# Optimization experiments

Measured on AMD Instinct MI355X. Metric: run time of the kernel, lower is better.

Reference implementation:

```python
import jax, jax.numpy as jnp
import numpy as np
from jax.scipy.special import logsumexp


def setup_inputs() -> dict:
    key = jax.random.key(0)
    B, C, H, W = 2, 32, 128, 128
    sizes = [(H, W)] + [(H // 2, W // 2)] * 4
    ks = iter(jax.random.split(key, 32))
    inp = {}
    for t, (hh, ww) in enumerate(sizes):
        inp[f"unary_h{t}"] = jax.random.normal(next(ks), (B, C, hh, ww), jnp.float32)
        inp[f"unary_v{t}"] = jax.random.normal(next(ks), (B, C, hh, ww), jnp.float32)
        inp[f"pairwise_h{t}"] = 0.1 * jax.random.normal(next(ks), (B, C, C, hh, ww - 1), jnp.float32)
        inp[f"pairwise_v{t}"] = 0.1 * jax.random.normal(next(ks), (B, C, C, hh - 1, ww), jnp.float32)
    inp["gamma"] = jnp.ones((1,), jnp.float32)
    return inp


def _chain_marginals(unary, pairwise, gamma):
    """Entropy-smoothed max-product marginals along the LAST axis.
    unary: [B,C,L,T], pairwise: [B,C,C,L,T-1] (pairwise[b,i,j,l,t] couples state i at t with j at t+1).
    Returns soft marginals [B,C,L,T] (softmax over C per position)."""
    u = jnp.transpose(unary, (3, 0, 2, 1))        # [T,B,L,C]
    pw = jnp.transpose(pairwise, (4, 0, 3, 1, 2))  # [T-1,B,L,C,C]
    inv_g = 1.0 / gamma

    def fwd_step(f, xs):
        u_t, pw_t = xs
        f_new = u_t + gamma * logsumexp(f[..., :, None] * inv_g + pw_t * inv_g, axis=-2)
        return f_new, f_new

    _, f_rest = jax.lax.scan(fwd_step, u[0], (u[1:], pw))
    f = jnp.concatenate([u[:1], f_rest], axis=0)

    def bwd_step(bb, xs):
        u_t, pw_t = xs
        b_new = u_t + gamma * logsumexp(bb[..., None, :] * inv_g + pw_t * inv_g, axis=-1)
        return b_new, b_new

    _, b_rest = jax.lax.scan(bwd_step, u[-1], (u[:-1][::-1], pw[::-1]))
    b = jnp.concatenate([u[-1:], b_rest], axis=0)[::-1]

    marg = jax.nn.softmax((f + b - u) * inv_g, axis=-1)  # [T,B,L,C]
    return jnp.transpose(marg, (1, 3, 2, 0))             # [B,C,L,T]


def _dp_pair(uh, uv, ph, pv, g):
    # horizontal chains (along W) with unary_h, vertical chains (along H) with unary_v
    mh = _chain_marginals(uh, ph, g)
    mv = _chain_marginals(uv.swapaxes(2, 3), pv.swapaxes(3, 4), g).swapaxes(2, 3)
    return mh, mv


def _scatter_up(m, stride, i, j, H, W):
    # max_unpool2d with the structured indices: m[y,x] -> (i + y*stride, j + x*stride), then crop/pad to (H,W)
    b, c, h_, w_ = m.shape
    up = jnp.zeros((b, c, h_ * stride, w_ * stride), m.dtype).at[:, :, i::stride, j::stride].set(m)
    up = up[:, :, :H, :W]
    ph, pw = H - up.shape[2], W - up.shape[3]
    if ph > 0 or pw > 0:
        up = jnp.pad(up, ((0, 0), (0, 0), (0, max(ph, 0)), (0, max(pw, 0))))
    return up


def reference(unary_h0, unary_h1, unary_h2, unary_h3, unary_h4,
              unary_v0, unary_v1, unary_v2, unary_v3, unary_v4,
              pairwise_h0, pairwise_h1, pairwise_h2, pairwise_h3, pairwise_h4,
              pairwise_v0, pairwise_v1, pairwise_v2, pairwise_v3, pairwise_v4,
              gamma):
    uh = [unary_h0, unary_h1, unary_h2, unary_h3, unary_h4]
    uv = [unary_v0, unary_v1, unary_v2, unary_v3, unary_v4]
    ph = [pairwise_h0, pairwise_h1, pairwise_h2, pairwise_h3, pairwise_h4]
    pv = [pairwise_v0, pairwise_v1, pairwise_v2, pairwise_v3, pairwise_v4]
    g = jnp.clip(gamma.reshape(()), 0.01)  # learned gamma, clamped min 0.01

    H, W = uh[0].shape[2], uh[0].shape[3]
    alpha = 1.0 / W if W > H else 1.0 / H

    mh0, mv0 = _dp_pair(uh[0], uv[0], ph[0], pv[0], g)
    marg_hs, marg_vs = [mh0], [mv0]
    mh_acc, mv_acc = mh0, mv0

    stride, cnt = 2, 1  # step_size = 1 default -> one extra scale with a 2x2 shifted grid
    for i in range(stride):
        for j in range(stride):
            m_h, m_v = _dp_pair(uh[cnt], uv[cnt], ph[cnt], pv[cnt], g)
            marg_hs.append(m_h)
            marg_vs.append(m_v)
            mh_acc = mh_acc + _scatter_up(m_h, stride, i, j, H, W)
            mv_acc = mv_acc + _scatter_up(m_v, stride, i, j, H, W)
            cnt += 1

    num_pairwise_terms = 2
    avg = (mh_acc + mv_acc) / (num_pairwise_terms * 2)

    new_uh0 = uh[0] - alpha * (marg_hs[0] - avg)
    new_uv0 = uv[0] - alpha * (marg_vs[0] - avg)
    # fine-scale unary updates (computed for faithfulness; gradients flow through avg)
    cnt = 1
    new_uh_fine, new_uv_fine = [], []
    for i in range(stride):
        for j in range(stride):
            new_uh_fine.append(uh[cnt] - alpha * (marg_hs[cnt] - avg[:, :, i::stride, j::stride]))
            new_uv_fine.append(uv[cnt] - alpha * (marg_vs[cnt] - avg[:, :, i::stride, j::stride]))
            cnt += 1

    main = jnp.stack([new_uh0, new_uv0, mh_acc, mv_acc], axis=0)  # [4,B,C,H,W]
    return main
```

## Files before the change

### kernel.cpp

```cpp
#include <hip/hip_runtime.h>
#include <stdint.h>

#define TC 2
#define CHUNK_BYTES 4096
#define CHUNK_F4 256

static __device__ __forceinline__ float lse16x2(const float* v, float igl2, float gln2, float uval)
{
  float a0=fmaxf(v[0],v[8]), a1=fmaxf(v[1],v[9]), a2=fmaxf(v[2],v[10]), a3=fmaxf(v[3],v[11]);
  float a4=fmaxf(v[4],v[12]),a5=fmaxf(v[5],v[13]),a6=fmaxf(v[6],v[14]),a7=fmaxf(v[7],v[15]);
  float b0=fmaxf(a0,a4), b1=fmaxf(a1,a5), b2=fmaxf(a2,a6), b3=fmaxf(a3,a7);
  float m = fmaxf(fmaxf(b0,b1), fmaxf(b2,b3));
  float e0 = exp2f((v[0]-m)*igl2) + exp2f((v[1]-m)*igl2);
  float e1 = exp2f((v[2]-m)*igl2) + exp2f((v[3]-m)*igl2);
  float e2 = exp2f((v[4]-m)*igl2) + exp2f((v[5]-m)*igl2);
  float e3 = exp2f((v[6]-m)*igl2) + exp2f((v[7]-m)*igl2);
  float e4 = exp2f((v[8]-m)*igl2) + exp2f((v[9]-m)*igl2);
  float e5 = exp2f((v[10]-m)*igl2) + exp2f((v[11]-m)*igl2);
  float e6 = exp2f((v[12]-m)*igl2) + exp2f((v[13]-m)*igl2);
  float e7 = exp2f((v[14]-m)*igl2) + exp2f((v[15]-m)*igl2);
  float s = ((e0+e1)+(e2+e3)) + ((e4+e5)+(e6+e7));
  float mo = __shfl_xor(m, 32);
  float m2 = fmaxf(m, mo);
  float sadj = s * exp2f((m - m2) * igl2);
  float stot = sadj + __shfl_xor(sadj, 32);
  return uval + m2 + gln2 * __log2f(stot);
}

static __device__ __forceinline__ float softmax32(float z)
{
  float zm = z;
  zm = fmaxf(zm, __shfl_xor(zm, 16));
  zm = fmaxf(zm, __shfl_xor(zm, 8));
  zm = fmaxf(zm, __shfl_xor(zm, 4));
  zm = fmaxf(zm, __shfl_xor(zm, 2));
  zm = fmaxf(zm, __shfl_xor(zm, 1));
  float p = exp2f((z - zm) * 1.4426950408889634f);
  float ps = p;
  ps += __shfl_xor(ps, 16);
  ps += __shfl_xor(ps, 8);
  ps += __shfl_xor(ps, 4);
  ps += __shfl_xor(ps, 2);
  ps += __shfl_xor(ps, 1);
  return p / ps;
}

static __device__ __forceinline__ uint32_t pkbf(float a, float b)
{
  uint32_t ua = __float_as_uint(a), ub = __float_as_uint(b);
  ua = (ua + 0x7FFFu + ((ua >> 16) & 1u)) >> 16;
  ub = (ub + 0x7FFFu + ((ub >> 16) & 1u)) & 0xFFFF0000u;
  return ua | ub;
}

struct TSeg { const float* pw; uint16_t* PT; int L, Tt, Tpad, fStride, Xtot, dirV, blockBase, nx, ny; };
struct TTable { TSeg s[10]; int nseg; };
struct USeg { const float* U; float* Ut; int fs, nx, ny, L, T, dirV, blockBase; };
struct UTable { USeg s[10]; int nseg; };
struct DSeg { const uint16_t* PT; const float* Ut; float* F; float* B; int chainBase, T, Tt, Tpad; };
struct DTable { DSeg s[10]; int nseg; };
struct MSeg { const float* F; const float* B; const float* Ut; float* out; int L, T, dirV, blockBase, nrx, nfx; };
struct MTable { MSeg s[10]; int nseg; };

__global__ __launch_bounds__(256) void k_transpose_all(TTable tbl)
{
  __shared__ uint16_t tile[128][128];
  int bid = blockIdx.x;
  int k = 0;
  for (int q = 1; q < tbl.nseg; q++) if (bid >= tbl.s[q].blockBase) k = q;
  TSeg sg = tbl.s[k];
  int r = bid - sg.blockBase;
  int jg = r & 7; r >>= 3;
  int w = r % sg.nx; int tmp = r / sg.nx;
  int fixed = tmp % sg.ny;
  int b = tmp / sg.ny;
  int j0 = jg * 4;
  int g = fixed * sg.fStride;
  int a = g & 31;
  int xbase = w * 128 - a;
  if (xbase >= sg.Xtot) return;
  int tid = threadIdx.x;
  int kx = tid & 31, psub = tid >> 5;
  int pstride = sg.L * sg.Tt;
  int clampMax = 2048 * pstride - 4;
  int jthr = j0 + (psub & 3);
  int swj = (jthr >> 1) & 3;
  int gp0 = ((psub >> 2) << 5) + jthr;
  int idx0 = ((b << 10) + gp0) * pstride + (g - a) + (w << 7) + (kx << 2);
  const float* pw = sg.pw;
  #pragma unroll
  for (int hp = 0; hp < 2; hp++) {
    float4 st[8];
    #pragma unroll
    for (int q = 0; q < 8; q++) {
      int batch = hp * 8 + q;
      int idx = idx0 + batch * (pstride << 6);
      idx = idx > clampMax ? clampMax : idx;
      st[q] = *(const float4*)(pw + idx);
    }
    #pragma unroll
    for (int q = 0; q < 8; q++) {
      int batch = hp * 8 + q;
      int i = 2 * batch + (psub >> 2);
      int sw = swj ^ (((i >> 3) & 3) << 2);
      int pl = batch * 8 + psub;
      uint32_t pk0 = pkbf(st[q].x, st[q].y);
      uint32_t pk1 = pkbf(st[q].z, st[q].w);
      if (sw & 1) { uint32_t tswp = pk0; pk0 = pk1; pk1 = tswp; }
      *(uint2*)((unsigned char*)tile + pl * 256 + 8 * (kx ^ (sw >> 1))) = make_uint2(pk0, pk1);
    }
  }
  __syncthreads();
  uint32_t* PTd = (uint32_t*)sg.PT;
  #pragma unroll
  for (int w8 = 0; w8 < 8; w8++) {
    int gidx = w8 * 256 + tid;
    int xs = gidx >> 4;
    int q = gidx & 15;
    int xv = xbase + xs;
    if (xv < 0 || xv >= sg.Xtot) continue;
    int jl = q >> 2, j = j0 + jl;
    int perm3 = (j >> 1) & 7;
    int swjW = (j >> 1) & 3;
    uint32_t pk[4];
    #pragma unroll
    for (int e = 0; e < 4; e++) {
      int wd = ((q & 3) << 2) + e;
      int pos = wd >> 1, pr = wd & 1;
      int i0 = ((pos ^ perm3) << 2) + pr * 2;
      int sw = swjW ^ (((i0 >> 3) & 3) << 2);
      int c = (xs >> 1) ^ sw;
      int u16c = (c << 1) | (xs & 1);
      int r0 = (i0 << 2) + jl;
      uint32_t v0 = tile[r0][u16c];
      uint32_t v1 = tile[r0 + 4][u16c];
      pk[e] = v0 | (v1 << 16);
    }
    int chain, tsl;
    if (sg.dirV) { chain = b * sg.Xtot + xv; tsl = fixed; }
    else         { chain = b * sg.ny + fixed; tsl = xv; }
    *(uint4*)&PTd[((size_t)chain * sg.Tpad + tsl) * 512 + j * 16 + (q & 3) * 4] =
        make_uint4(pk[0], pk[1], pk[2], pk[3]);
  }
}

__global__ __launch_bounds__(256) void k_ut_all(UTable tbl)
{
  __shared__ float tile[32][33];
  int bid = blockIdx.x;
  int k = 0;
  for (int q = 1; q < tbl.nseg; q++) if (bid >= tbl.s[q].blockBase) k = q;
  USeg sg = tbl.s[k];
  int r = bid - sg.blockBase;
  int bx = r % sg.nx; int tmp = r / sg.nx;
  int fixed = tmp % sg.ny;
  int b = tmp / sg.ny;
  int tid = threadIdx.x;
  size_t LT = (size_t)sg.L * sg.T;
  int x0 = bx * 32;
  int xx = tid & 31;
  #pragma unroll
  for (int it = 0; it < 4; it++) {
    int c = (tid >> 5) + it * 8;
    tile[xx][c] = sg.U[(size_t)b * 32 * LT + (size_t)c * LT + (size_t)fixed * sg.fs + x0 + xx];
  }
  __syncthreads();
  int xw = tid >> 3;
  int ci = (tid & 7) * 4;
  int chain = sg.dirV ? b * sg.L + x0 + xw : b * sg.L + fixed;
  int tIdx  = sg.dirV ? fixed : x0 + xw;
  float4 vv = make_float4(tile[xw][ci], tile[xw][ci + 1], tile[xw][ci + 2], tile[xw][ci + 3]);
  *(float4*)&sg.Ut[((size_t)chain * sg.T + tIdx) * 32 + ci] = vv;
}

__global__ __launch_bounds__(64) void k_dp_all(DTable tbl, const float* __restrict__ gamma, int nDP)
{
  __shared__ __align__(16) unsigned char lds[2 * CHUNK_BYTES + 1024];
  float* f_out = (float*)(lds + 2 * CHUNK_BYTES);
  int bid = blockIdx.x;
  int isB = (bid >= nDP) ? 1 : 0;
  bid -= isB * nDP;
  int k = 0;
  for (int q = 1; q < tbl.nseg; q++) if (bid >= tbl.s[q].chainBase) k = q;
  DSeg sg = tbl.s[k];
  int chain = bid - sg.chainBase;
  int T = sg.T, Tt = sg.Tt;
  int tid = threadIdx.x, j = tid & 31, h = tid >> 5;
  float g = fmaxf(gamma[0], 0.01f);
  float igl2 = (1.0f / g) * 1.4426950408889634f;
  float gln2 = g * 0.6931471805599453f;
  const float* Utc = sg.Ut + (size_t)chain * T * 32;
  float* Oc = (isB ? sg.B : sg.F) + (size_t)chain * T * 32;
  const float4* src = (const float4*)(sg.PT + (size_t)chain * sg.Tpad * 1024);
  int nch = sg.Tpad / TC;
  int perm3 = (j >> 1) & 7;
  int gbase = h * 48;
  float4 stg[4];
  if (!isB) {
    float cur = Utc[j];
    if (h == 0) f_out[j] = cur;
    #pragma unroll
    for (int q = 0; q < 4; q++) stg[q] = src[q * 64 + tid];
    int buf = 0;
    for (int ch = 0; ch < nch; ch++) {
      float4* dst = (float4*)(lds + buf * CHUNK_BYTES);
      #pragma unroll
      for (int q = 0; q < 4; q++) dst[q * 64 + tid] = stg[q];
      if (ch + 1 < nch) {
        const float4* s2 = src + (size_t)(ch + 1) * CHUNK_F4;
        #pragma unroll
        for (int q = 0; q < 4; q++) stg[q] = s2[q * 64 + tid];
      }
      #pragma unroll
      for (int ss = 0; ss < TC; ss++) {
        int s = ch * TC + ss;
        if (s >= Tt) break;
        const uint32_t* sl = (const uint32_t*)(lds + buf * CHUNK_BYTES + ss * 2048);
        float v[16];
        #pragma unroll
        for (int rr = 0; rr < 4; rr++) {
          int pos = (4 * h + rr) ^ perm3;
          uint2 dv = *(const uint2*)&sl[j * 16 + pos * 2];
          v[rr * 4 + 0] = __uint_as_float(dv.x << 16);
          v[rr * 4 + 1] = __uint_as_float(dv.x & 0xFFFF0000u);
          v[rr * 4 + 2] = __uint_as_float(dv.y << 16);
          v[rr * 4 + 3] = __uint_as_float(dv.y & 0xFFFF0000u);
        }
        #pragma unroll
        for (int q = 0; q < 16; q++) v[q] += __shfl(cur, gbase + q);
        int t = s + 1;
        float uval = Utc[(size_t)t * 32 + j];
        cur = lse16x2(v, igl2, gln2, uval);
        if (h == 0) f_out[(t & 7) * 32 + j] = cur;
        if ((t & 7) == 7) {
          float4 vv = *(float4*)&f_out[tid * 4];
          *(float4*)&Oc[(size_t)(t - 7) * 32 + tid * 4] = vv;
        }
      }
      buf ^= 1;
    }
  } else {
    int p2i = j >> 2, pri = (j >> 1) & 1, loi = j & 1;
    float cur = Utc[(size_t)(T - 1) * 32 + j];
    if (h == 0) f_out[7 * 32 + j] = cur;
    {
      const float4* s2 = src + (size_t)(nch - 1) * CHUNK_F4;
      #pragma unroll
      for (int q = 0; q < 4; q++) stg[q] = s2[q * 64 + tid];
    }
    int buf = 0;
    for (int ch = nch - 1; ch >= 0; ch--) {
      float4* dst = (float4*)(lds + buf * CHUNK_BYTES);
      #pragma unroll
      for (int q = 0; q < 4; q++) dst[q * 64 + tid] = stg[q];
      if (ch > 0) {
        const float4* s2 = src + (size_t)(ch - 1) * CHUNK_F4;
        #pragma unroll
        for (int q = 0; q < 4; q++) stg[q] = s2[q * 64 + tid];
      }
      #pragma unroll
      for (int ss = TC - 1; ss >= 0; ss--) {
        int s = ch * TC + ss;
        if (s >= Tt) continue;
        const uint16_t* row16 = (const uint16_t*)(lds + buf * CHUNK_BYTES + ss * 2048);
        float v[16];
        #pragma unroll
        for (int jj = 0; jj < 16; jj++) {
          int u16idx = (16 * h + jj) * 32 + ((p2i ^ (jj >> 1)) * 2 + pri) * 2 + loi;
          v[jj] = __uint_as_float((uint32_t)row16[u16idx] << 16);
        }
        #pragma unroll
        for (int q = 0; q < 16; q++) v[q] += __shfl(cur, gbase + q);
        float uval = Utc[(size_t)s * 32 + j];
        cur = lse16x2(v, igl2, gln2, uval);
        if (h == 0) f_out[(s & 7) * 32 + j] = cur;
        if ((s & 7) == 0) {
          float4 vv = *(float4*)&f_out[tid * 4];
          *(float4*)&Oc[(size_t)s * 32 + tid * 4] = vv;
        }
      }
      buf ^= 1;
    }
  }
}

__global__ __launch_bounds__(256) void k_marg_all(MTable tbl, const float* __restrict__ gamma)
{
  __shared__ float sm[32][33];
  int bid = blockIdx.x;
  int k = 0;
  for (int q = 1; q < tbl.nseg; q++) if (bid >= tbl.s[q].blockBase) k = q;
  MSeg sg = tbl.s[k];
  int r = bid - sg.blockBase;
  int rx = r % sg.nrx; int tmp = r / sg.nrx;
  int fx = tmp % sg.nfx; int b = tmp / sg.nfx;
  int tid = threadIdx.x;
  float g = fmaxf(gamma[0], 0.01f);
  float ig = 1.0f / g;
  int c = tid & 31;
  int L = sg.L, T = sg.T;
  size_t LT = (size_t)L * T;
  int RA = sg.dirV ? L : T;
  int r0 = rx * 32;
  #pragma unroll
  for (int pass = 0; pass < 4; pass++) {
    int rr = (tid >> 5) + pass * 8;
    int rowAxis = r0 + rr;
    int chain = sg.dirV ? b * L + rowAxis : b * L + fx;
    int t = sg.dirV ? fx : rowAxis;
    size_t idx = ((size_t)chain * T + t) * 32 + c;
    float z = (sg.F[idx] + sg.B[idx] - sg.Ut[idx]) * ig;
    sm[rr][c] = softmax32(z);
  }
  __syncthreads();
  int cc = tid >> 3;
  int xl = (tid & 7) * 4;
  size_t obase = (size_t)b * 32 * LT + (size_t)fx * RA + r0;
  float4 vv = make_float4(sm[xl][cc], sm[xl + 1][cc], sm[xl + 2][cc], sm[xl + 3][cc]);
  *(float4*)&sg.out[obase + (size_t)cc * LT + xl] = vv;
}

__global__ __launch_bounds__(256) void k_combine(
    const float* __restrict__ uh0, const float* __restrict__ uv0,
    const float* __restrict__ MB, float* __restrict__ out)
{
  int t4 = blockIdx.x * 256 + threadIdx.x;
  int base = t4 * 4;
  int x = base & 127, y = (base >> 7) & 127;
  int bc = base >> 14;
  float4 mh0 = *(const float4*)&MB[base];
  float4 mv0 = *(const float4*)&MB[1048576 + base];
  int ce = 1 + ((y & 1) << 1);
  int coff = bc * 4096 + ((y >> 1) << 6) + (x >> 1);
  const float* cbE = MB + 2097152 + (size_t)(ce - 1) * 524288;
  const float* cbO = cbE + 524288;
  float2 mhcE = *(const float2*)&cbE[coff];
  float2 mhcO = *(const float2*)&cbO[coff];
  float2 mvcE = *(const float2*)&cbE[262144 + coff];
  float2 mvcO = *(const float2*)&cbO[262144 + coff];
  float4 u_h = *(const float4*)&uh0[base];
  float4 u_v = *(const float4*)&uv0[base];
  float mh[4] = {mh0.x, mh0.y, mh0.z, mh0.w};
  float mv[4] = {mv0.x, mv0.y, mv0.z, mv0.w};
  float uh[4] = {u_h.x, u_h.y, u_h.z, u_h.w};
  float uv[4] = {u_v.x, u_v.y, u_v.z, u_v.w};
  float mhc[4] = {mhcE.x, mhcO.x, mhcE.y, mhcO.y};
  float mvc[4] = {mvcE.x, mvcO.x, mvcE.y, mvcO.y};
  float o0[4], o1[4], o2[4], o3[4];
  const float A = 0.0078125f;
  #pragma unroll
  for (int e = 0; e < 4; e++) {
    float mha = mh[e] + mhc[e], mva = mv[e] + mvc[e];
    float avg = (mha + mva) * 0.25f;
    o0[e] = uh[e] - A * (mh[e] - avg);
    o1[e] = uv[e] - A * (mv[e] - avg);
    o2[e] = mha; o3[e] = mva;
  }
  *(float4*)&out[base]           = make_float4(o0[0], o0[1], o0[2], o0[3]);
  *(float4*)&out[1048576 + base] = make_float4(o1[0], o1[1], o1[2], o1[3]);
  *(float4*)&out[2097152 + base] = make_float4(o2[0], o2[1], o2[2], o2[3]);
  *(float4*)&out[3145728 + base] = make_float4(o3[0], o3[1], o3[2], o3[3]);
}

static void fill_tseg(TSeg& t, const float* pw, uint16_t* PT, int L, int T, int dirV, int blockBase)
{
  int Tt = T - 1;
  t.pw = pw; t.PT = PT;
  t.L = L; t.Tt = Tt; t.Tpad = T;
  t.fStride = dirV ? L : Tt;
  t.Xtot = dirV ? L : Tt;
  t.dirV = dirV;
  int pad = (t.fStride & 31) ? 31 : 0;
  t.nx = (t.Xtot + pad + 127) / 128;
  t.ny = dirV ? Tt : L;
  t.blockBase = blockBase;
}

extern "C" void kernel_launch(void* const* d_in, const int* in_sizes, int n_in,
                              void* d_out, int out_size, void* d_ws, size_t ws_size,
                              hipStream_t stream)
{
  (void)in_sizes; (void)n_in; (void)out_size;
  const float* gamma = (const float*)d_in[20];
  unsigned char* ws = (unsigned char*)d_ws;

  int segL[10], segT[10];
  const float* segPW[10]; const float* segUU[10];
  size_t segMG[10];
  for (int lvl = 0; lvl < 5; lvl++) {
    int H = lvl ? 64 : 128, W = H;
    int si = lvl * 2;
    segL[si] = H; segT[si] = W;
    segPW[si] = (const float*)d_in[lvl * 4 + 2];
    segUU[si] = (const float*)d_in[lvl * 4 + 0];
    segL[si + 1] = W; segT[si + 1] = H;
    segPW[si + 1] = (const float*)d_in[lvl * 4 + 3];
    segUU[si + 1] = (const float*)d_in[lvl * 4 + 1];
    if (lvl == 0) { segMG[0] = 0; segMG[1] = 1048576; }
    else { segMG[si] = 2097152 + (size_t)(lvl - 1) * 524288; segMG[si + 1] = segMG[si] + 262144; }
  }

  const size_t NEED = 318767104ull;
  if (ws_size >= NEED) {
    uint16_t* PT0 = (uint16_t*)ws;
    float* MARG = (float*)ws;
    float* F0  = (float*)(ws + 268435456ull);
    float* B0  = (float*)(ws + 285212672ull);
    float* Ut0 = (float*)(ws + 301989888ull);

    TTable tt; UTable ut; DTable dt; MTable mt;
    tt.nseg = 10; ut.nseg = 10; dt.nseg = 10; mt.nseg = 10;
    size_t ptOff = 0, fuOff = 0;
    int tB = 0, uB = 0, cB = 0, mB = 0;
    for (int s = 0; s < 10; s++) {
      int dirV = s & 1;
      int L = segL[s], T = segT[s];
      int chains = 2 * L;
      fill_tseg(tt.s[s], segPW[s], PT0 + ptOff, L, T, dirV, tB);
      tB += 2 * tt.s[s].ny * tt.s[s].nx * 8;
      USeg& u = ut.s[s];
      u.U = segUU[s]; u.Ut = Ut0 + fuOff;
      u.fs = dirV ? L : T;
      u.nx = (dirV ? L : T) / 32;
      u.ny = dirV ? T : L;
      u.L = L; u.T = T; u.dirV = dirV;
      u.blockBase = uB;
      uB += u.nx * u.ny * 2;
      DSeg& d = dt.s[s];
      d.PT = PT0 + ptOff; d.Ut = Ut0 + fuOff;
      d.F = F0 + fuOff; d.B = B0 + fuOff;
      d.chainBase = cB; d.T = T; d.Tt = T - 1; d.Tpad = T;
      cB += chains;
      MSeg& m = mt.s[s];
      m.F = F0 + fuOff; m.B = B0 + fuOff; m.Ut = Ut0 + fuOff;
      m.out = MARG + segMG[s];
      m.L = L; m.T = T; m.dirV = dirV;
      m.blockBase = mB;
      m.nrx = (dirV ? L : T) / 32;
      m.nfx = dirV ? T : L;
      mB += 2 * m.nfx * m.nrx;
      ptOff += (size_t)chains * T * 1024;
      fuOff += (size_t)chains * T * 32;
    }
    k_transpose_all<<<tB, 256, 0, stream>>>(tt);
    k_ut_all<<<uB, 256, 0, stream>>>(ut);
    k_dp_all<<<2 * cB, 64, 0, stream>>>(dt, gamma, cB);
    k_marg_all<<<mB, 256, 0, stream>>>(mt, gamma);
    k_combine<<<1024, 256, 0, stream>>>((const float*)d_in[0], (const float*)d_in[1],
                                        MARG, (float*)d_out);
  } else {
    uint16_t* PT0 = (uint16_t*)ws;
    float* F0  = (float*)(ws + 67108864ull);
    float* B0  = (float*)(ws + 71303168ull);
    float* Ut0 = (float*)(ws + 75497472ull);
    float* MARG = (float*)(ws + 79691776ull);
    for (int s = 0; s < 10; s++) {
      int dirV = s & 1;
      int L = segL[s], T = segT[s];
      int chains = 2 * L;
      TTable tt; tt.nseg = 1;
      fill_tseg(tt.s[0], segPW[s], PT0, L, T, dirV, 0);
      int nb = 2 * tt.s[0].ny * tt.s[0].nx * 8;
      k_transpose_all<<<nb, 256, 0, stream>>>(tt);
      UTable ut; ut.nseg = 1;
      USeg& u = ut.s[0];
      u.U = segUU[s]; u.Ut = Ut0;
      u.fs = dirV ? L : T;
      u.nx = (dirV ? L : T) / 32;
      u.ny = dirV ? T : L;
      u.L = L; u.T = T; u.dirV = dirV; u.blockBase = 0;
      int ub = u.nx * u.ny * 2;
      k_ut_all<<<ub, 256, 0, stream>>>(ut);
      DTable dt; dt.nseg = 1;
      DSeg& d = dt.s[0];
      d.PT = PT0; d.Ut = Ut0; d.F = F0; d.B = B0;
      d.chainBase = 0; d.T = T; d.Tt = T - 1; d.Tpad = T;
      k_dp_all<<<2 * chains, 64, 0, stream>>>(dt, gamma, chains);
      MTable mt; mt.nseg = 1;
      MSeg& m = mt.s[0];
      m.F = F0; m.B = B0; m.Ut = Ut0; m.out = MARG + segMG[s];
      m.L = L; m.T = T; m.dirV = dirV; m.blockBase = 0;
      m.nrx = (dirV ? L : T) / 32;
      m.nfx = dirV ? T : L;
      int mb = 2 * m.nfx * m.nrx;
      k_marg_all<<<mb, 256, 0, stream>>>(mt, gamma);
    }
    k_combine<<<1024, 256, 0, stream>>>((const float*)d_in[0], (const float*)d_in[1],
                                        MARG, (float*)d_out);
  }
}
```

Measured before the change: 426.7 us.

## Fuse forward and backward DP passes per block and pre-scale into log2 domain

The forward and backward recursions of each chain now run interleaved in one 64-thread block instead of in separate blocks, sharing a doubled LDS double-buffer, so two independent dependency chains hide each other's latency. The 1/gamma*log2e scaling is also folded into the pairwise transpose (before bf16 packing) and the unary transpose, which removes the multiplies from the lse and softmax inner loops. This halves the grid, so fewer blocks run with more work each; it also changes bf16 rounding because values are scaled before quantization.

```diff
diff --git a/kernel.cpp b/kernel.cpp
--- a/kernel.cpp
+++ b/kernel.cpp
@@ -5,29 +5,29 @@
 #define CHUNK_BYTES 4096
 #define CHUNK_F4 256
 
-static __device__ __forceinline__ float lse16x2(const float* v, float igl2, float gln2, float uval)
+static __device__ __forceinline__ float lse16x2_l2(const float* v, float uval)
 {
   float a0=fmaxf(v[0],v[8]), a1=fmaxf(v[1],v[9]), a2=fmaxf(v[2],v[10]), a3=fmaxf(v[3],v[11]);
   float a4=fmaxf(v[4],v[12]),a5=fmaxf(v[5],v[13]),a6=fmaxf(v[6],v[14]),a7=fmaxf(v[7],v[15]);
   float b0=fmaxf(a0,a4), b1=fmaxf(a1,a5), b2=fmaxf(a2,a6), b3=fmaxf(a3,a7);
   float m = fmaxf(fmaxf(b0,b1), fmaxf(b2,b3));
-  float e0 = exp2f((v[0]-m)*igl2) + exp2f((v[1]-m)*igl2);
-  float e1 = exp2f((v[2]-m)*igl2) + exp2f((v[3]-m)*igl2);
-  float e2 = exp2f((v[4]-m)*igl2) + exp2f((v[5]-m)*igl2);
-  float e3 = exp2f((v[6]-m)*igl2) + exp2f((v[7]-m)*igl2);
-  float e4 = exp2f((v[8]-m)*igl2) + exp2f((v[9]-m)*igl2);
-  float e5 = exp2f((v[10]-m)*igl2) + exp2f((v[11]-m)*igl2);
-  float e6 = exp2f((v[12]-m)*igl2) + exp2f((v[13]-m)*igl2);
-  float e7 = exp2f((v[14]-m)*igl2) + exp2f((v[15]-m)*igl2);
+  float e0 = exp2f(v[0]-m) + exp2f(v[1]-m);
+  float e1 = exp2f(v[2]-m) + exp2f(v[3]-m);
+  float e2 = exp2f(v[4]-m) + exp2f(v[5]-m);
+  float e3 = exp2f(v[6]-m) + exp2f(v[7]-m);
+  float e4 = exp2f(v[8]-m) + exp2f(v[9]-m);
+  float e5 = exp2f(v[10]-m) + exp2f(v[11]-m);
+  float e6 = exp2f(v[12]-m) + exp2f(v[13]-m);
+  float e7 = exp2f(v[14]-m) + exp2f(v[15]-m);
   float s = ((e0+e1)+(e2+e3)) + ((e4+e5)+(e6+e7));
   float mo = __shfl_xor(m, 32);
   float m2 = fmaxf(m, mo);
-  float sadj = s * exp2f((m - m2) * igl2);
+  float sadj = s * exp2f(m - m2);
   float stot = sadj + __shfl_xor(sadj, 32);
-  return uval + m2 + gln2 * __log2f(stot);
-}
-
-static __device__ __forceinline__ float softmax32(float z)
+  return uval + m2 + __log2f(stot);
+}
+
+static __device__ __forceinline__ float softmax32_l2(float z)
 {
   float zm = z;
   zm = fmaxf(zm, __shfl_xor(zm, 16));
@@ -35,7 +35,7 @@
   zm = fmaxf(zm, __shfl_xor(zm, 4));
   zm = fmaxf(zm, __shfl_xor(zm, 2));
   zm = fmaxf(zm, __shfl_xor(zm, 1));
-  float p = exp2f((z - zm) * 1.4426950408889634f);
+  float p = exp2f(z - zm);
   float ps = p;
   ps += __shfl_xor(ps, 16);
   ps += __shfl_xor(ps, 8);
@@ -62,13 +62,14 @@
 struct MSeg { const float* F; const float* B; const float* Ut; float* out; int L, T, dirV, blockBase, nrx, nfx; };
 struct MTable { MSeg s[10]; int nseg; };
 
-__global__ __launch_bounds__(256) void k_transpose_all(TTable tbl)
+__global__ __launch_bounds__(256) void k_transpose_all(TTable tbl, const float* __restrict__ gamma)
 {
   __shared__ uint16_t tile[128][128];
   int bid = blockIdx.x;
   int k = 0;
   for (int q = 1; q < tbl.nseg; q++) if (bid >= tbl.s[q].blockBase) k = q;
   TSeg sg = tbl.s[k];
+  float igl2 = 1.4426950408889634f / fmaxf(gamma[0], 0.01f);
   int r = bid - sg.blockBase;
   int jg = r & 7; r >>= 3;
   int w = r % sg.nx; int tmp = r / sg.nx;
@@ -104,8 +105,8 @@
       int i = 2 * batch + (psub >> 2);
       int sw = swj ^ (((i >> 3) & 3) << 2);
       int pl = batch * 8 + psub;
-      uint32_t pk0 = pkbf(st[q].x, st[q].y);
-      uint32_t pk1 = pkbf(st[q].z, st[q].w);
+      uint32_t pk0 = pkbf(st[q].x * igl2, st[q].y * igl2);
+      uint32_t pk1 = pkbf(st[q].z * igl2, st[q].w * igl2);
       if (sw & 1) { uint32_t tswp = pk0; pk0 = pk1; pk1 = tswp; }
       *(uint2*)((unsigned char*)tile + pl * 256 + 8 * (kx ^ (sw >> 1))) = make_uint2(pk0, pk1);
     }
@@ -144,13 +145,14 @@
   }
 }
 
-__global__ __launch_bounds__(256) void k_ut_all(UTable tbl)
+__global__ __launch_bounds__(256) void k_ut_all(UTable tbl, const float* __restrict__ gamma)
 {
   __shared__ float tile[32][33];
   int bid = blockIdx.x;
   int k = 0;
   for (int q = 1; q < tbl.nseg; q++) if (bid >= tbl.s[q].blockBase) k = q;
   USeg sg = tbl.s[k];
+  float igl2 = 1.4426950408889634f / fmaxf(gamma[0], 0.01f);
   int r = bid - sg.blockBase;
   int bx = r % sg.nx; int tmp = r / sg.nx;
   int fixed = tmp % sg.ny;
@@ -169,122 +171,116 @@
   int ci = (tid & 7) * 4;
   int chain = sg.dirV ? b * sg.L + x0 + xw : b * sg.L + fixed;
   int tIdx  = sg.dirV ? fixed : x0 + xw;
-  float4 vv = make_float4(tile[xw][ci], tile[xw][ci + 1], tile[xw][ci + 2], tile[xw][ci + 3]);
+  float4 vv = make_float4(tile[xw][ci] * igl2, tile[xw][ci + 1] * igl2,
+                          tile[xw][ci + 2] * igl2, tile[xw][ci + 3] * igl2);
   *(float4*)&sg.Ut[((size_t)chain * sg.T + tIdx) * 32 + ci] = vv;
 }
 
-__global__ __launch_bounds__(64) void k_dp_all(DTable tbl, const float* __restrict__ gamma, int nDP)
-{
-  __shared__ __align__(16) unsigned char lds[2 * CHUNK_BYTES + 1024];
-  float* f_out = (float*)(lds + 2 * CHUNK_BYTES);
+__global__ __launch_bounds__(64) void k_dp_all(DTable tbl)
+{
+  __shared__ __align__(16) unsigned char lds[4 * CHUNK_BYTES + 2048];
+  float* fF_out = (float*)(lds + 4 * CHUNK_BYTES);
+  float* fB_out = fF_out + 256;
   int bid = blockIdx.x;
-  int isB = (bid >= nDP) ? 1 : 0;
-  bid -= isB * nDP;
   int k = 0;
   for (int q = 1; q < tbl.nseg; q++) if (bid >= tbl.s[q].chainBase) k = q;
   DSeg sg = tbl.s[k];
   int chain = bid - sg.chainBase;
   int T = sg.T, Tt = sg.Tt;
   int tid = threadIdx.x, j = tid & 31, h = tid >> 5;
-  float g = fmaxf(gamma[0], 0.01f);
-  float igl2 = (1.0f / g) * 1.4426950408889634f;
-  float gln2 = g * 0.6931471805599453f;
   const float* Utc = sg.Ut + (size_t)chain * T * 32;
-  float* Oc = (isB ? sg.B : sg.F) + (size_t)chain * T * 32;
+  float* Fc = sg.F + (size_t)chain * T * 32;
+  float* Bc = sg.B + (size_t)chain * T * 32;
   const float4* src = (const float4*)(sg.PT + (size_t)chain * sg.Tpad * 1024);
   int nch = sg.Tpad / TC;
   int perm3 = (j >> 1) & 7;
   int gbase = h * 48;
-  float4 stg[4];
-  if (!isB) {
-    float cur = Utc[j];
-    if (h == 0) f_out[j] = cur;
-    #pragma unroll
-    for (int q = 0; q < 4; q++) stg[q] = src[q * 64 + tid];
-    int buf = 0;
-    for (int ch = 0; ch < nch; ch++) {
-      float4* dst = (float4*)(lds + buf * CHUNK_BYTES);
+  int p2i = j >> 2, pri = (j >> 1) & 1, loi = j & 1;
+  float curF = Utc[j];
+  float curB = Utc[(size_t)(T - 1) * 32 + j];
+  if (h == 0) { fF_out[j] = curF; fB_out[7 * 32 + j] = curB; }
+  float4 stgF[4], stgB[4];
+  #pragma unroll
+  for (int q = 0; q < 4; q++) stgF[q] = src[q * 64 + tid];
+  {
+    const float4* s2 = src + (size_t)(nch - 1) * CHUNK_F4;
+    #pragma unroll
+    for (int q = 0; q < 4; q++) stgB[q] = s2[q * 64 + tid];
+  }
+  for (int ch = 0; ch < nch; ch++) {
+    int bc = nch - 1 - ch;
+    unsigned char* bufF = lds + (ch & 1) * CHUNK_BYTES;
+    unsigned char* bufB = lds + 2 * CHUNK_BYTES + (ch & 1) * CHUNK_BYTES;
+    float4* dF = (float4*)bufF;
+    float4* dB = (float4*)bufB;
+    #pragma unroll
+    for (int q = 0; q < 4; q++) { dF[q * 64 + tid] = stgF[q]; dB[q * 64 + tid] = stgB[q]; }
+    if (ch + 1 < nch) {
+      const float4* sF2 = src + (size_t)(ch + 1) * CHUNK_F4;
+      const float4* sB2 = src + (size_t)(bc - 1) * CHUNK_F4;
       #pragma unroll
-      for (int q = 0; q < 4; q++) dst[q * 64 + tid] = stg[q];
-      if (ch + 1 < nch) {
-        const float4* s2 = src + (size_t)(ch + 1) * CHUNK_F4;
-        #pragma unroll
-        for (int q = 0; q < 4; q++) stg[q] = s2[q * 64 + tid];
-      }
-      #pragma unroll
-      for (int ss = 0; ss < TC; ss++) {
-        int s = ch * TC + ss;
-        if (s >= Tt) break;
-        const uint32_t* sl = (const uint32_t*)(lds + buf * CHUNK_BYTES + ss * 2048);
-        float v[16];
+      for (int q = 0; q < 4; q++) { stgF[q] = sF2[q * 64 + tid]; stgB[q] = sB2[q * 64 + tid]; }
+    }
+    #pragma unroll
+    for (int ss = 0; ss < TC; ss++) {
+      int sF = ch * TC + ss;
+      int sB = bc * TC + (TC - 1 - ss);
+      bool doF = sF < Tt;
+      bool doB = sB < Tt;
+      int tF = doF ? (sF + 1) : 0;
+      int tB = doB ? sB : 0;
+      float uF = Utc[(size_t)tF * 32 + j];
+      float uB = Utc[(size_t)tB * 32 + j];
+      float vF[16];
+      {
+        const uint32_t* sl = (const uint32_t*)(bufF + ss * 2048);
         #pragma unroll
         for (int rr = 0; rr < 4; rr++) {
           int pos = (4 * h + rr) ^ perm3;
           uint2 dv = *(const uint2*)&sl[j * 16 + pos * 2];
-          v[rr * 4 + 0] = __uint_as_float(dv.x << 16);
-          v[rr * 4 + 1] = __uint_as_float(dv.x & 0xFFFF0000u);
-          v[rr * 4 + 2] = __uint_as_float(dv.y << 16);
-          v[rr * 4 + 3] = __uint_as_float(dv.y & 0xFFFF0000u);
+          vF[rr * 4 + 0] = __uint_as_float(dv.x << 16);
+          vF[rr * 4 + 1] = __uint_as_float(dv.x & 0xFFFF0000u);
+          vF[rr * 4 + 2] = __uint_as_float(dv.y << 16);
+          vF[rr * 4 + 3] = __uint_as_float(dv.y & 0xFFFF0000u);
         }
-        #pragma unroll
-        for (int q = 0; q < 16; q++) v[q] += __shfl(cur, gbase + q);
-        int t = s + 1;
-        float uval = Utc[(size_t)t * 32 + j];
-        cur = lse16x2(v, igl2, gln2, uval);
-        if (h == 0) f_out[(t & 7) * 32 + j] = cur;
-        if ((t & 7) == 7) {
-          float4 vv = *(float4*)&f_out[tid * 4];
-          *(float4*)&Oc[(size_t)(t - 7) * 32 + tid * 4] = vv;
-        }
-      }
-      buf ^= 1;
-    }
-  } else {
-    int p2i = j >> 2, pri = (j >> 1) & 1, loi = j & 1;
-    float cur = Utc[(size_t)(T - 1) * 32 + j];
-    if (h == 0) f_out[7 * 32 + j] = cur;
-    {
-      const float4* s2 = src + (size_t)(nch - 1) * CHUNK_F4;
-      #pragma unroll
-      for (int q = 0; q < 4; q++) stg[q] = s2[q * 64 + tid];
-    }
-    int buf = 0;
-    for (int ch = nch - 1; ch >= 0; ch--) {
-      float4* dst = (float4*)(lds + buf * CHUNK_BYTES);
-      #pragma unroll
-      for (int q = 0; q < 4; q++) dst[q * 64 + tid] = stg[q];
-      if (ch > 0) {
-        const float4* s2 = src + (size_t)(ch - 1) * CHUNK_F4;
-        #pragma unroll
-        for (int q = 0; q < 4; q++) stg[q] = s2[q * 64 + tid];
-      }
-      #pragma unroll
-      for (int ss = TC - 1; ss >= 0; ss--) {
-        int s = ch * TC + ss;
-        if (s >= Tt) continue;
-        const uint16_t* row16 = (const uint16_t*)(lds + buf * CHUNK_BYTES + ss * 2048);
-        float v[16];
+      }
+      float vB[16];
+      {
+        const uint16_t* row16 = (const uint16_t*)(bufB + (TC - 1 - ss) * 2048);
         #pragma unroll
         for (int jj = 0; jj < 16; jj++) {
           int u16idx = (16 * h + jj) * 32 + ((p2i ^ (jj >> 1)) * 2 + pri) * 2 + loi;
-          v[jj] = __uint_as_float((uint32_t)row16[u16idx] << 16);
+          vB[jj] = __uint_as_float((uint32_t)row16[u16idx] << 16);
         }
-        #pragma unroll
-        for (int q = 0; q < 16; q++) v[q] += __shfl(cur, gbase + q);
-        float uval = Utc[(size_t)s * 32 + j];
-        cur = lse16x2(v, igl2, gln2, uval);
-        if (h == 0) f_out[(s & 7) * 32 + j] = cur;
-        if ((s & 7) == 0) {
-          float4 vv = *(float4*)&f_out[tid * 4];
-          *(float4*)&Oc[(size_t)s * 32 + tid * 4] = vv;
-        }
-      }
-      buf ^= 1;
-    }
-  }
-}
-
-__global__ __launch_bounds__(256) void k_marg_all(MTable tbl, const float* __restrict__ gamma)
+      }
+      #pragma unroll
+      for (int q = 0; q < 16; q++) {
+        vF[q] += __shfl(curF, gbase + q);
+        vB[q] += __shfl(curB, gbase + q);
+      }
+      float nF = lse16x2_l2(vF, uF);
+      float nB = lse16x2_l2(vB, uB);
+      if (doF) {
+        curF = nF;
+        if (h == 0) fF_out[(tF & 7) * 32 + j] = curF;
+      }
+      if (doB) {
+        curB = nB;
+        if (h == 0) fB_out[(tB & 7) * 32 + j] = curB;
+      }
+      if (doF && (tF & 7) == 7) {
+        float4 vv = *(float4*)&fF_out[tid * 4];
+        *(float4*)&Fc[(size_t)(tF - 7) * 32 + tid * 4] = vv;
+      }
+      if (doB && (tB & 7) == 0) {
+        float4 vv = *(float4*)&fB_out[tid * 4];
+        *(float4*)&Bc[(size_t)tB * 32 + tid * 4] = vv;
+      }
+    }
+  }
+}
+
+__global__ __launch_bounds__(256) void k_marg_all(MTable tbl)
 {
   __shared__ float sm[32][33];
   int bid = blockIdx.x;
@@ -295,8 +291,6 @@
   int rx = r % sg.nrx; int tmp = r / sg.nrx;
   int fx = tmp % sg.nfx; int b = tmp / sg.nfx;
   int tid = threadIdx.x;
-  float g = fmaxf(gamma[0], 0.01f);
-  float ig = 1.0f / g;
   int c = tid & 31;
   int L = sg.L, T = sg.T;
   size_t LT = (size_t)L * T;
@@ -309,8 +303,8 @@
     int chain = sg.dirV ? b * L + rowAxis : b * L + fx;
     int t = sg.dirV ? fx : rowAxis;
     size_t idx = ((size_t)chain * T + t) * 32 + c;
-    float z = (sg.F[idx] + sg.B[idx] - sg.Ut[idx]) * ig;
-    sm[rr][c] = softmax32(z);
+    float z = sg.F[idx] + sg.B[idx] - sg.Ut[idx];
+    sm[rr][c] = softmax32_l2(z);
   }
   __syncthreads();
   int cc = tid >> 3;
@@ -442,10 +436,10 @@
       ptOff += (size_t)chains * T * 1024;
       fuOff += (size_t)chains * T * 32;
     }
-    k_transpose_all<<<tB, 256, 0, stream>>>(tt);
-    k_ut_all<<<uB, 256, 0, stream>>>(ut);
-    k_dp_all<<<2 * cB, 64, 0, stream>>>(dt, gamma, cB);
-    k_marg_all<<<mB, 256, 0, stream>>>(mt, gamma);
+    k_transpose_all<<<tB, 256, 0, stream>>>(tt, gamma);
+    k_ut_all<<<uB, 256, 0, stream>>>(ut, gamma);
+    k_dp_all<<<cB, 64, 0, stream>>>(dt);
+    k_marg_all<<<mB, 256, 0, stream>>>(mt);
     k_combine<<<1024, 256, 0, stream>>>((const float*)d_in[0], (const float*)d_in[1],
                                         MARG, (float*)d_out);
   } else {
@@ -461,7 +455,7 @@
       TTable tt; tt.nseg = 1;
       fill_tseg(tt.s[0], segPW[s], PT0, L, T, dirV, 0);
       int nb = 2 * tt.s[0].ny * tt.s[0].nx * 8;
-      k_transpose_all<<<nb, 256, 0, stream>>>(tt);
+      k_transpose_all<<<nb, 256, 0, stream>>>(tt, gamma);
       UTable ut; ut.nseg = 1;
       USeg& u = ut.s[0];
       u.U = segUU[s]; u.Ut = Ut0;
@@ -470,12 +464,12 @@
       u.ny = dirV ? T : L;
       u.L = L; u.T = T; u.dirV = dirV; u.blockBase = 0;
       int ub = u.nx * u.ny * 2;
-      k_ut_all<<<ub, 256, 0, stream>>>(ut);
+      k_ut_all<<<ub, 256, 0, stream>>>(ut, gamma);
       DTable dt; dt.nseg = 1;
       DSeg& d = dt.s[0];
       d.PT = PT0; d.Ut = Ut0; d.F = F0; d.B = B0;
       d.chainBase = 0; d.T = T; d.Tt = T - 1; d.Tpad = T;
-      k_dp_all<<<2 * chains, 64, 0, stream>>>(dt, gamma, chains);
+      k_dp_all<<<chains, 64, 0, stream>>>(dt);
       MTable mt; mt.nseg = 1;
       MSeg& m = mt.s[0];
       m.F = F0; m.B = B0; m.Ut = Ut0; m.out = MARG + segMG[s];
@@ -483,7 +477,7 @@
       m.nrx = (dirV ? L : T) / 32;
       m.nfx = dirV ? T : L;
       int mb = 2 * m.nfx * m.nrx;
-      k_marg_all<<<mb, 256, 0, stream>>>(mt, gamma);
+      k_marg_all<<<mb, 256, 0, stream>>>(mt);
     }
     k_combine<<<1024, 256, 0, stream>>>((const float*)d_in[0], (const float*)d_in[1],
                                         MARG, (float*)d_out);
```

Result: slower. 466.2 us (+9.2%).
